# Kernel tuning notes

Measured on AMD Instinct MI355X. Metric: run time of the kernel, lower is better.

The kernel has to match this reference:

```python
import jax, jax.numpy as jnp
import numpy as np
from jax import lax

NUM_HEADS = 8
EPS = 1e-12  # F.normalize default eps


def setup_inputs() -> dict:
    key = jax.random.key(0)
    k1, k2, k3, k4 = jax.random.split(key, 4)
    b, c, h, w, d = 2, 128, 48, 48, 48
    x = jax.random.normal(k1, (b, c, h, w, d), dtype=jnp.float32)
    qkv_w = jax.random.normal(k2, (3 * c, c), dtype=jnp.float32) * 0.05
    dw_w = jax.random.normal(k3, (3 * c, 1, 3, 3, 3), dtype=jnp.float32) * 0.05
    proj_w = jax.random.normal(k4, (c, c), dtype=jnp.float32) * 0.05
    temperature = jnp.ones((1, NUM_HEADS, 1, 1), dtype=jnp.float32)
    return {"x": x, "qkv_w": qkv_w, "dw_w": dw_w, "proj_w": proj_w,
            "temperature": temperature}


def _l2_normalize(t):
    # F.normalize(t, dim=-1): t / max(||t||_2, eps)
    n = jnp.sqrt(jnp.sum(t * t, axis=-1, keepdims=True))
    return t / jnp.maximum(n, EPS)


def reference(x, qkv_w, dw_w, proj_w, temperature):
    b, c, h, w, d = x.shape
    dh = c // NUM_HEADS
    N = h * w * d
    # 1x1x1 pointwise conv (c -> 3c), no bias: pure channel GEMM
    qkv = jnp.einsum('oc,bchwd->bohwd', qkv_w, x)
    # depthwise 3x3x3 conv, padding=1, groups=3c
    qkv = lax.conv_general_dilated(
        qkv, dw_w, window_strides=(1, 1, 1), padding=[(1, 1)] * 3,
        dimension_numbers=('NCDHW', 'OIDHW', 'NCDHW'),
        feature_group_count=3 * c)
    q, k, v = jnp.split(qkv, 3, axis=1)
    q = q.reshape(b, NUM_HEADS, dh, N)
    k = k.reshape(b, NUM_HEADS, dh, N)
    v = v.reshape(b, NUM_HEADS, dh, N)
    q = _l2_normalize(q)
    k = _l2_normalize(k)
    # transposed attention: [b,H,dh,dh] score matrix over channels
    attn = jnp.einsum('bhin,bhjn->bhij', q, k) * temperature
    attn = jax.nn.softmax(attn, axis=-1)
    out = jnp.einsum('bhij,bhjn->bhin', attn, v).reshape(b, c, h, w, d)
    # 1x1x1 projection (c -> c), no bias
    return jnp.einsum('oc,bchwd->bohwd', proj_w, out)
```

## Files before the change

### kernel.cpp

```cpp
#include <hip/hip_runtime.h>
#include <hip/hip_bf16.h>
#include <stdint.h>
#include <stddef.h>

#define NSP 110592
#define SD  48
#define SD2 2304
#define CIN 128
#define C3  384
#define NH  8
#define NB  2
#define NQ  84934656ull

typedef __hip_bfloat16 bf16;
typedef __bf16 bf16x8 __attribute__((ext_vector_type(8)));
typedef float  f32x4  __attribute__((ext_vector_type(4)));

#define WOFF_QKVW 0
#define WOFF_DWW  49152
#define WOFF_PROJ 59520
#define WOFF_TEMP 75904
#define WTOTAL    75912

__device__ __forceinline__ float ldb(const bf16* p){ return __bfloat162float(*p); }
__device__ __forceinline__ float b2f(uint16_t u){
    union { float f; uint32_t i; } x; x.i = (uint32_t)u << 16; return x.f;
}
__device__ __forceinline__ uint16_t f2b(float f){
    bf16 h = __float2bfloat16(f); return *(uint16_t*)&h;
}

__global__ void k_sniff(const uint16_t* __restrict__ x16, int* __restrict__ flag)
{
    int t = threadIdx.x; int cnt = 0;
    for (int i = 0; i < 16; ++i) {
        uint16_t b = x16[(size_t)(t * 16 + i) * 2];
        int e = (b >> 7) & 0xFF;
        if (e >= 100 && e <= 140) ++cnt;
    }
    for (int off = 32; off; off >>= 1) cnt += __shfl_down(cnt, off, 64);
    __shared__ int s[4];
    if ((t & 63) == 0) s[t >> 6] = cnt;
    __syncthreads();
    if (t == 0) *flag = (s[0] + s[1] + s[2] + s[3] < 2048) ? 1 : 0;
}

__global__ void k_cvtw(const void* __restrict__ qw, const void* __restrict__ dw,
                       const void* __restrict__ pw, const void* __restrict__ tw,
                       bf16* __restrict__ wbuf, const int* __restrict__ flagp)
{
    int f = *flagp;
    int idx = blockIdx.x * 256 + threadIdx.x;
    if (idx >= WTOTAL) return;
    const void* src; int off;
    if (idx < WOFF_DWW)      { src = qw; off = idx; }
    else if (idx < WOFF_PROJ){ src = dw; off = idx - WOFF_DWW; }
    else if (idx < WOFF_TEMP){ src = pw; off = idx - WOFF_PROJ; }
    else                     { src = tw; off = idx - WOFF_TEMP; }
    float v = f ? ((const float*)src)[off]
                : __bfloat162float(((const bf16*)src)[off]);
    wbuf[idx] = __float2bfloat16(v);
}

__global__ __launch_bounds__(256) void k_transpose(const void* __restrict__ xin,
                                                   bf16* __restrict__ xT,
                                                   const int* __restrict__ flagp)
{
    int f = *flagp;
    int b = blockIdx.y;
    size_t tid = (size_t)blockIdx.x * 256 + threadIdx.x;
    int c = (int)(tid & 127);
    size_t n8 = tid >> 7;
    size_t base = ((size_t)b * CIN + c) * NSP + n8 * 8;
    bf16 pv[8];
    if (f) {
        const float* src = (const float*)xin + base;
        float4 a = *(const float4*)src;
        float4 d = *(const float4*)(src + 4);
        pv[0] = __float2bfloat16(a.x); pv[1] = __float2bfloat16(a.y);
        pv[2] = __float2bfloat16(a.z); pv[3] = __float2bfloat16(a.w);
        pv[4] = __float2bfloat16(d.x); pv[5] = __float2bfloat16(d.y);
        pv[6] = __float2bfloat16(d.z); pv[7] = __float2bfloat16(d.w);
    } else {
        uint4 v = *(const uint4*)((const bf16*)xin + base);
        const bf16* q = (const bf16*)&v;
#pragma unroll
        for (int j = 0; j < 8; ++j) pv[j] = q[j];
    }
    bf16* dst = xT + ((size_t)b * NSP + n8 * 8) * CIN + c;
#pragma unroll
    for (int j = 0; j < 8; ++j) dst[(size_t)j * CIN] = pv[j];
}

__global__ __launch_bounds__(256) void k_gemm_bt(const bf16* __restrict__ A,
                                                 const bf16* __restrict__ BT,
                                                 void* __restrict__ Cout,
                                                 int Mtotal,
                                                 const int* __restrict__ flagp,
                                                 int mblocks)
{
    __shared__ __align__(16) bf16 lA[128 * CIN];
    __shared__ __align__(16) bf16 lB[128 * CIN];
    int b = blockIdx.z;
    int bx = blockIdx.x;
    int mb, nb;
    if (mblocks == 3) {
        int g = bx / 24, w = bx % 24;
        nb = g * 8 + (w & 7);
        mb = w >> 3;
    } else { mb = 0; nb = bx; }
    size_t nbase = (size_t)nb * 128;
    const bf16* gA = A + (size_t)mb * 128 * CIN;
    const bf16* gB = BT + ((size_t)b * NSP + nbase) * CIN;
    int t = threadIdx.x;
#pragma unroll
    for (int i = 0; i < 8; ++i) {
        int off = (i * 256 + t) * 8;
        *(uint4*)&lA[off] = *(const uint4*)&gA[off];
        *(uint4*)&lB[off] = *(const uint4*)&gB[off];
    }
    __syncthreads();

    int wave = t >> 6, lane = t & 63;
    int wm = (wave & 1) * 64, wn = (wave >> 1) * 64;
    int lr = lane & 15, lq = lane >> 4;
    f32x4 acc[4][4];
#pragma unroll
    for (int mi = 0; mi < 4; ++mi)
#pragma unroll
        for (int ni = 0; ni < 4; ++ni) acc[mi][ni] = (f32x4){0.f, 0.f, 0.f, 0.f};

#pragma unroll
    for (int ks = 0; ks < 4; ++ks) {
        int kof = ks * 32 + lq * 8;
        bf16x8 af[4], bfv[4];
#pragma unroll
        for (int mi = 0; mi < 4; ++mi)
            af[mi] = *(const bf16x8*)&lA[(wm + mi * 16 + lr) * CIN + kof];
#pragma unroll
        for (int ni = 0; ni < 4; ++ni)
            bfv[ni] = *(const bf16x8*)&lB[(wn + ni * 16 + lr) * CIN + kof];
#pragma unroll
        for (int mi = 0; mi < 4; ++mi)
#pragma unroll
            for (int ni = 0; ni < 4; ++ni)
                acc[mi][ni] = __builtin_amdgcn_mfma_f32_16x16x32_bf16(
                    af[mi], bfv[ni], acc[mi][ni], 0, 0, 0);
    }

    int f32o = flagp ? *flagp : 0;
    size_t cb = ((size_t)b * Mtotal + (size_t)mb * 128) * NSP + nbase;
    if (f32o) {
        float* Cb = (float*)Cout + cb;
#pragma unroll
        for (int mi = 0; mi < 4; ++mi)
#pragma unroll
            for (int ni = 0; ni < 4; ++ni)
#pragma unroll
                for (int r = 0; r < 4; ++r)
                    Cb[(size_t)(wm + mi * 16 + lq * 4 + r) * NSP + wn + ni * 16 + lr]
                        = acc[mi][ni][r];
    } else {
        bf16* Cb = (bf16*)Cout + cb;
#pragma unroll
        for (int mi = 0; mi < 4; ++mi)
#pragma unroll
            for (int ni = 0; ni < 4; ++ni)
#pragma unroll
                for (int r = 0; r < 4; ++r)
                    Cb[(size_t)(wm + mi * 16 + lq * 4 + r) * NSP + wn + ni * 16 + lr]
                        = __float2bfloat16(acc[mi][ni][r]);
    }
}

#define PLN 3200
__global__ __launch_bounds__(256) void k_dwconv(const bf16* __restrict__ qkv1,
                                                const bf16* __restrict__ dw,
                                                bf16* __restrict__ qkv2,
                                                float* __restrict__ sums)
{
    __shared__ __align__(16) bf16 lds[8 * PLN];
    __shared__ float red[4];
    int bc = blockIdx.x;
    int slab = blockIdx.y;
    int z0 = slab * 6;
    int ch = bc % C3;
    int t = threadIdx.x;
    const bf16* src = qkv1 + (size_t)bc * NSP;
    bf16* dst = qkv2 + (size_t)bc * NSP;

    float wgt[27];
#pragma unroll
    for (int i = 0; i < 27; ++i) wgt[i] = ldb(&dw[ch * 27 + i]);

#pragma unroll
    for (int i = 0; i < 13; ++i) {
        int idx = i * 256 + t;
        if (idx < 3200) *(uint4*)&lds[idx * 8] = (uint4){0, 0, 0, 0};
    }
    __syncthreads();

#pragma unroll
    for (int i = 0; i < 9; ++i) {
        int vidx = i * 256 + t;
        int p = vidx / 288;
        int r = vidx - p * 288;
        int y = r / 6;
        int dg = r - y * 6;
        int zp = z0 - 1 + p;
        if ((unsigned)zp < SD) {
            uint4 v = *(const uint4*)&src[(size_t)zp * SD2 + y * SD + dg * 8];
            *(uint4*)&lds[(p * PLN + (y + 1) * 64 + 8 + dg * 8)] = v;
        }
    }
    __syncthreads();

    float ssq = 0.f;
#pragma unroll 1
    for (int r = 0; r < 3; ++r) {
        int s = r * 256 + t;
        if (s < 576) {
            int y = s / 12;
            int c4 = (s - y * 12) * 4;
            float acc[6][4];
#pragma unroll
            for (int oz = 0; oz < 6; ++oz)
#pragma unroll
                for (int d = 0; d < 4; ++d) acc[oz][d] = 0.f;

#pragma unroll
            for (int pl = 0; pl < 8; ++pl) {
                const uint16_t* P =
                    (const uint16_t*)lds + pl * PLN + y * 64 + 8 + c4;
                float v[3][6];
#pragma unroll
                for (int dy = 0; dy < 3; ++dy) {
                    const uint16_t* R = P + dy * 64;
                    uint2 m = *(const uint2*)R;
                    v[dy][0] = b2f(R[-1]);
                    v[dy][1] = b2f((uint16_t)m.x);
                    v[dy][2] = b2f((uint16_t)(m.x >> 16));
                    v[dy][3] = b2f((uint16_t)m.y);
                    v[dy][4] = b2f((uint16_t)(m.y >> 16));
                    v[dy][5] = b2f(R[4]);
                }
                float p0[4] = {0.f,0.f,0.f,0.f};
                float p1[4] = {0.f,0.f,0.f,0.f};
                float p2[4] = {0.f,0.f,0.f,0.f};
#pragma unroll
                for (int dy = 0; dy < 3; ++dy)
#pragma unroll
                    for (int dd = 0; dd < 3; ++dd) {
                        float w0 = wgt[dy * 3 + dd];
                        float w1 = wgt[9 + dy * 3 + dd];
                        float w2 = wgt[18 + dy * 3 + dd];
#pragma unroll
                        for (int d = 0; d < 4; ++d) {
                            float xv = v[dy][d + dd];
                            if (pl <= 5)            p0[d] += w0 * xv;
                            if (pl >= 1 && pl <= 6) p1[d] += w1 * xv;
                            if (pl >= 2)            p2[d] += w2 * xv;
                        }
                    }
#pragma unroll
                for (int d = 0; d < 4; ++d) {
                    if (pl <= 5)            acc[pl][d]     += p0[d];
                    if (pl >= 1 && pl <= 6) acc[pl - 1][d] += p1[d];
                    if (pl >= 2)            acc[pl - 2][d] += p2[d];
                }
            }
#pragma unroll
            for (int oz = 0; oz < 6; ++oz) {
                uint16_t u0 = f2b(acc[oz][0]), u1 = f2b(acc[oz][1]);
                uint16_t u2 = f2b(acc[oz][2]), u3 = f2b(acc[oz][3]);
                uint2 o;
                o.x = (uint32_t)u0 | ((uint32_t)u1 << 16);
                o.y = (uint32_t)u2 | ((uint32_t)u3 << 16);
                *(uint2*)&dst[(size_t)(z0 + oz) * SD2 + y * SD + c4] = o;
#pragma unroll
                for (int d = 0; d < 4; ++d) ssq += acc[oz][d] * acc[oz][d];
            }
        }
    }

    for (int off = 32; off; off >>= 1) ssq += __shfl_down(ssq, off, 64);
    if ((t & 63) == 0) red[t >> 6] = ssq;
    __syncthreads();
    if (t == 0) atomicAdd(&sums[bc], red[0] + red[1] + red[2] + red[3]);
}

__global__ __launch_bounds__(256) void k_scores(const bf16* __restrict__ qkv2,
                                                float* __restrict__ scores)
{
    int b = blockIdx.z, h = blockIdx.y;
    const bf16* qb = qkv2 + ((size_t)b * C3 + h * 16) * NSP;
    const bf16* kb = qkv2 + ((size_t)b * C3 + 128 + h * 16) * NSP;
    int t = threadIdx.x, w = t >> 6, lane = t & 63;
    int m = lane & 15, q4 = lane >> 4;
    size_t n0 = (size_t)blockIdx.x * 1024 + (size_t)w * 256 + (size_t)q4 * 8;
    const bf16* qp = qb + (size_t)m * NSP + n0;
    const bf16* kp = kb + (size_t)m * NSP + n0;
    f32x4 acc = (f32x4){0.f, 0.f, 0.f, 0.f};
#pragma unroll
    for (int it = 0; it < 8; ++it) {
        bf16x8 a  = *(const bf16x8*)(qp + it * 32);
        bf16x8 bb = *(const bf16x8*)(kp + it * 32);
        acc = __builtin_amdgcn_mfma_f32_16x16x32_bf16(a, bb, acc, 0, 0, 0);
    }
    float* srow = scores + (size_t)(b * NH + h) * 256;
#pragma unroll
    for (int r = 0; r < 4; ++r)
        atomicAdd(&srow[(q4 * 4 + r) * 16 + m], acc[r]);
}

__global__ void k_softmax(const float* __restrict__ scores,
                          const float* __restrict__ sums,
                          const bf16* __restrict__ temp,
                          float* __restrict__ attn)
{
    int t = threadIdx.x;
    int h = (t >> 4) & 7, b = t >> 7;
    float tau = __bfloat162float(temp[h]);
    float invq = 1.f / fmaxf(sqrtf(sums[b * C3 + (t & 127)]), 1e-12f);
    const float* srow = scores + (size_t)t * 16;
    float s[16]; float mx = -3.4e38f;
#pragma unroll
    for (int j = 0; j < 16; ++j) {
        float invk = 1.f / fmaxf(sqrtf(sums[b * C3 + 128 + h * 16 + j]), 1e-12f);
        s[j] = srow[j] * invq * invk * tau;
        mx = fmaxf(mx, s[j]);
    }
    float sum = 0.f;
#pragma unroll
    for (int j = 0; j < 16; ++j) { s[j] = expf(s[j] - mx); sum += s[j]; }
    float inv = 1.f / sum;
    float* arow = attn + (size_t)t * 16;
#pragma unroll
    for (int j = 0; j < 16; ++j) arow[j] = s[j] * inv;
}

__global__ __launch_bounds__(256) void k_av(const bf16* __restrict__ qkv2,
                                            const float* __restrict__ attn,
                                            bf16* __restrict__ outT)
{
    int b = blockIdx.z, h = blockIdx.y;
    const bf16* vb = qkv2 + ((size_t)b * C3 + 256 + h * 16) * NSP;
    __shared__ float at[256];
    int t = threadIdx.x;
    {
        int i = t >> 4, j = t & 15;
        at[j * 16 + i] = attn[(size_t)(b * NH + h) * 256 + t];
    }
    __syncthreads();
    size_t n0 = (size_t)blockIdx.x * 1024 + (size_t)t * 4;
    float acc[16][4];
#pragma unroll
    for (int i = 0; i < 16; ++i)
#pragma unroll
        for (int k = 0; k < 4; ++k) acc[i][k] = 0.f;
#pragma unroll
    for (int j = 0; j < 16; ++j) {
        uint2 raw = *(const uint2*)&vb[(size_t)j * NSP + n0];
        const bf16* rp = (const bf16*)&raw;
        float vf[4];
#pragma unroll
        for (int k = 0; k < 4; ++k) vf[k] = ldb(&rp[k]);
#pragma unroll
        for (int i = 0; i < 16; ++i) {
            float wv = at[j * 16 + i];
#pragma unroll
            for (int k = 0; k < 4; ++k) acc[i][k] += wv * vf[k];
        }
    }
    bf16* ob = outT + ((size_t)b * NSP + n0) * CIN + h * 16;
#pragma unroll
    for (int k = 0; k < 4; ++k) {
        bf16 tmp[16];
#pragma unroll
        for (int i = 0; i < 16; ++i) tmp[i] = __float2bfloat16(acc[i][k]);
        *(uint4*)&ob[(size_t)k * CIN]     = *(uint4*)&tmp[0];
        *(uint4*)&ob[(size_t)k * CIN + 8] = *(uint4*)&tmp[8];
    }
}

extern "C" void kernel_launch(void* const* d_in, const int* in_sizes, int n_in,
                              void* d_out, int out_size, void* d_ws, size_t ws_size,
                              hipStream_t stream)
{
    const void *px = nullptr, *pq = nullptr, *pd = nullptr, *pp = nullptr, *pt = nullptr;
    for (int i = 0; i < n_in; ++i) {
        switch (in_sizes[i]) {
            case 28311552: px = d_in[i]; break;
            case 49152:    pq = d_in[i]; break;
            case 10368:    pd = d_in[i]; break;
            case 16384:    pp = d_in[i]; break;
            case 8:        pt = d_in[i]; break;
        }
    }
    const size_t required = NQ * 4 + (1u << 20);
    if (!px || !pq || !pd || !pp || !pt || ws_size < required) {
        (void)hipMemsetAsync(d_out, 0, (size_t)out_size * 2, stream);
        return;
    }

    char* ws = (char*)d_ws;
    bf16* qkv1 = (bf16*)ws;
    bf16* qkv2 = (bf16*)(ws + NQ * 2);
    char* small = ws + NQ * 4;
    int*   flag   = (int*)small;
    float* sums   = (float*)(small + 256);
    float* scores = (float*)(small + 8192);
    float* attn   = (float*)(small + 24576);
    bf16*  wbuf   = (bf16*)(small + 40960);
    bf16* xT   = qkv2;
    bf16* outT = qkv1;

    (void)hipMemsetAsync(small, 0, 40960, stream);
    k_sniff<<<1, 256, 0, stream>>>((const uint16_t*)px, flag);
    k_cvtw<<<(WTOTAL + 255) / 256, 256, 0, stream>>>(pq, pd, pp, pt, wbuf, flag);
    k_transpose<<<dim3(6912, NB), 256, 0, stream>>>(px, xT, flag);
    k_gemm_bt<<<dim3(864 * 3, 1, NB), 256, 0, stream>>>(
        wbuf + WOFF_QKVW, xT, qkv1, C3, nullptr, 3);
    k_dwconv<<<dim3(NB * C3, 8), 256, 0, stream>>>(qkv1, wbuf + WOFF_DWW, qkv2, sums);
    k_scores<<<dim3(108, NH, NB), 256, 0, stream>>>(qkv2, scores);
    k_softmax<<<1, 256, 0, stream>>>(scores, sums, wbuf + WOFF_TEMP, attn);
    k_av<<<dim3(108, NH, NB), 256, 0, stream>>>(qkv2, attn, outT);
    k_gemm_bt<<<dim3(864, 1, NB), 256, 0, stream>>>(
        wbuf + WOFF_PROJ, outT, d_out, CIN, flag, 1);
}
```

Before: 552.0 us.

## Rework depthwise conv with packed FMA, swizzled LDS, smaller z-slabs

```diff
diff --git a/kernel.cpp b/kernel.cpp
--- a/kernel.cpp
+++ b/kernel.cpp
@@ -15,6 +15,7 @@
 typedef __hip_bfloat16 bf16;
 typedef __bf16 bf16x8 __attribute__((ext_vector_type(8)));
 typedef float  f32x4  __attribute__((ext_vector_type(4)));
+typedef float  f32x2  __attribute__((ext_vector_type(2)));
 
 #define WOFF_QKVW 0
 #define WOFF_DWW  49152
@@ -28,6 +29,12 @@
 }
 __device__ __forceinline__ uint16_t f2b(float f){
     bf16 h = __float2bfloat16(f); return *(uint16_t*)&h;
+}
+__device__ __forceinline__ float blo(uint32_t u){
+    union { float f; uint32_t i; } x; x.i = u << 16; return x.f;
+}
+__device__ __forceinline__ float bhi(uint32_t u){
+    union { float f; uint32_t i; } x; x.i = u & 0xffff0000u; return x.f;
 }
 
 __global__ void k_sniff(const uint16_t* __restrict__ x16, int* __restrict__ flag)
@@ -174,16 +181,17 @@
 }
 
 #define PLN 3200
-__global__ __launch_bounds__(256) void k_dwconv(const bf16* __restrict__ qkv1,
-                                                const bf16* __restrict__ dw,
-                                                bf16* __restrict__ qkv2,
-                                                float* __restrict__ sums)
-{
-    __shared__ __align__(16) bf16 lds[8 * PLN];
+#define PLB 6400
+__global__ __launch_bounds__(256, 4) void k_dwconv(const bf16* __restrict__ qkv1,
+                                                   const bf16* __restrict__ dw,
+                                                   bf16* __restrict__ qkv2,
+                                                   float* __restrict__ sums)
+{
+    __shared__ __align__(16) bf16 lds[6 * PLN];
     __shared__ float red[4];
     int bc = blockIdx.x;
     int slab = blockIdx.y;
-    int z0 = slab * 6;
+    int z0 = slab * 4;
     int ch = bc % C3;
     int t = threadIdx.x;
     const bf16* src = qkv1 + (size_t)bc * NSP;
@@ -194,95 +202,112 @@
     for (int i = 0; i < 27; ++i) wgt[i] = ldb(&dw[ch * 27 + i]);
 
 #pragma unroll
-    for (int i = 0; i < 13; ++i) {
+    for (int i = 0; i < 10; ++i) {
         int idx = i * 256 + t;
-        if (idx < 3200) *(uint4*)&lds[idx * 8] = (uint4){0, 0, 0, 0};
-    }
-    __syncthreads();
-
-#pragma unroll
-    for (int i = 0; i < 9; ++i) {
+        if (idx < 2400) *(uint4*)&lds[idx * 8] = (uint4){0, 0, 0, 0};
+    }
+    __syncthreads();
+
+#pragma unroll
+    for (int i = 0; i < 7; ++i) {
         int vidx = i * 256 + t;
-        int p = vidx / 288;
-        int r = vidx - p * 288;
-        int y = r / 6;
-        int dg = r - y * 6;
-        int zp = z0 - 1 + p;
-        if ((unsigned)zp < SD) {
-            uint4 v = *(const uint4*)&src[(size_t)zp * SD2 + y * SD + dg * 8];
-            *(uint4*)&lds[(p * PLN + (y + 1) * 64 + 8 + dg * 8)] = v;
+        if (vidx < 1728) {
+            int p = vidx / 288;
+            int rr = vidx - p * 288;
+            int yy = rr / 6;
+            int dg = rr - yy * 6;
+            int zp = z0 - 1 + p;
+            if ((unsigned)zp < SD) {
+                uint4 v = *(const uint4*)&src[(size_t)zp * SD2 + yy * SD + dg * 8];
+                int ab = p * PLB + (yy + 1) * 128 + 16 + dg * 16;
+                ab ^= ((yy + 1) & 7) << 4;
+                *(uint4*)((char*)lds + ab) = v;
+            }
         }
     }
     __syncthreads();
 
-    float ssq = 0.f;
+    f32x2 ss2 = (f32x2){0.f, 0.f};
 #pragma unroll 1
-    for (int r = 0; r < 3; ++r) {
+    for (int r = 0; r < 2; ++r) {
         int s = r * 256 + t;
-        if (s < 576) {
-            int y = s / 12;
-            int c4 = (s - y * 12) * 4;
-            float acc[6][4];
-#pragma unroll
-            for (int oz = 0; oz < 6; ++oz)
-#pragma unroll
-                for (int d = 0; d < 4; ++d) acc[oz][d] = 0.f;
-
-#pragma unroll
-            for (int pl = 0; pl < 8; ++pl) {
-                const uint16_t* P =
-                    (const uint16_t*)lds + pl * PLN + y * 64 + 8 + c4;
-                float v[3][6];
+        if (s < 288) {
+            int y = s / 6;
+            int c8 = (s - y * 6) * 8;
+            int offL[3], offM[3], offR[3];
+#pragma unroll
+            for (int dy = 0; dy < 3; ++dy) {
+                int row = y + dy;
+                int sw = (row & 7) << 4;
+                int rb = row * 128 + 2 * c8;
+                offL[dy] = (rb + 12) ^ sw;
+                offM[dy] = (rb + 16) ^ sw;
+                offR[dy] = (rb + 32) ^ sw;
+            }
+            f32x2 acc2[4][4];
+#pragma unroll
+            for (int oz = 0; oz < 4; ++oz)
+#pragma unroll
+                for (int m = 0; m < 4; ++m) acc2[oz][m] = (f32x2){0.f, 0.f};
+
+            const char* ldsb = (const char*)lds;
+#pragma unroll
+            for (int pl = 0; pl < 6; ++pl) {
+                const char* Pb = ldsb + pl * PLB;
 #pragma unroll
                 for (int dy = 0; dy < 3; ++dy) {
-                    const uint16_t* R = P + dy * 64;
-                    uint2 m = *(const uint2*)R;
-                    v[dy][0] = b2f(R[-1]);
-                    v[dy][1] = b2f((uint16_t)m.x);
-                    v[dy][2] = b2f((uint16_t)(m.x >> 16));
-                    v[dy][3] = b2f((uint16_t)m.y);
-                    v[dy][4] = b2f((uint16_t)(m.y >> 16));
-                    v[dy][5] = b2f(R[4]);
-                }
-                float p0[4] = {0.f,0.f,0.f,0.f};
-                float p1[4] = {0.f,0.f,0.f,0.f};
-                float p2[4] = {0.f,0.f,0.f,0.f};
-#pragma unroll
-                for (int dy = 0; dy < 3; ++dy)
-#pragma unroll
-                    for (int dd = 0; dd < 3; ++dd) {
-                        float w0 = wgt[dy * 3 + dd];
-                        float w1 = wgt[9 + dy * 3 + dd];
-                        float w2 = wgt[18 + dy * 3 + dd];
-#pragma unroll
-                        for (int d = 0; d < 4; ++d) {
-                            float xv = v[dy][d + dd];
-                            if (pl <= 5)            p0[d] += w0 * xv;
-                            if (pl >= 1 && pl <= 6) p1[d] += w1 * xv;
-                            if (pl >= 2)            p2[d] += w2 * xv;
-                        }
+                    uint32_t Lw = *(const uint32_t*)(Pb + offL[dy]);
+                    uint4    Mw = *(const uint4*)   (Pb + offM[dy]);
+                    uint32_t Rw = *(const uint32_t*)(Pb + offR[dy]);
+                    f32x2 vb0 = (f32x2){blo(Mw.x), bhi(Mw.x)};
+                    f32x2 vb1 = (f32x2){blo(Mw.y), bhi(Mw.y)};
+                    f32x2 vb2 = (f32x2){blo(Mw.z), bhi(Mw.z)};
+                    f32x2 vb3 = (f32x2){blo(Mw.w), bhi(Mw.w)};
+                    f32x2 va0 = (f32x2){bhi(Lw),   blo(Mw.x)};
+                    f32x2 va1 = (f32x2){bhi(Mw.x), blo(Mw.y)};
+                    f32x2 va2 = (f32x2){bhi(Mw.y), blo(Mw.z)};
+                    f32x2 va3 = (f32x2){bhi(Mw.z), blo(Mw.w)};
+                    f32x2 va4 = (f32x2){bhi(Mw.w), blo(Rw)};
+#pragma unroll
+                    for (int wp = 0; wp < 3; ++wp) {
+                        int oz = pl - wp;
+                        if (oz < 0 || oz > 3) continue;
+                        int wb = wp * 9 + dy * 3;
+                        float w0 = wgt[wb], w1 = wgt[wb + 1], w2 = wgt[wb + 2];
+                        f32x2 w0p = (f32x2){w0, w0};
+                        f32x2 w1p = (f32x2){w1, w1};
+                        f32x2 w2p = (f32x2){w2, w2};
+                        acc2[oz][0] = __builtin_elementwise_fma(va0, w0p, acc2[oz][0]);
+                        acc2[oz][1] = __builtin_elementwise_fma(va1, w0p, acc2[oz][1]);
+                        acc2[oz][2] = __builtin_elementwise_fma(va2, w0p, acc2[oz][2]);
+                        acc2[oz][3] = __builtin_elementwise_fma(va3, w0p, acc2[oz][3]);
+                        acc2[oz][0] = __builtin_elementwise_fma(vb0, w1p, acc2[oz][0]);
+                        acc2[oz][1] = __builtin_elementwise_fma(vb1, w1p, acc2[oz][1]);
+                        acc2[oz][2] = __builtin_elementwise_fma(vb2, w1p, acc2[oz][2]);
+                        acc2[oz][3] = __builtin_elementwise_fma(vb3, w1p, acc2[oz][3]);
+                        acc2[oz][0] = __builtin_elementwise_fma(va1, w2p, acc2[oz][0]);
+                        acc2[oz][1] = __builtin_elementwise_fma(va2, w2p, acc2[oz][1]);
+                        acc2[oz][2] = __builtin_elementwise_fma(va3, w2p, acc2[oz][2]);
+                        acc2[oz][3] = __builtin_elementwise_fma(va4, w2p, acc2[oz][3]);
                     }
-#pragma unroll
-                for (int d = 0; d < 4; ++d) {
-                    if (pl <= 5)            acc[pl][d]     += p0[d];
-                    if (pl >= 1 && pl <= 6) acc[pl - 1][d] += p1[d];
-                    if (pl >= 2)            acc[pl - 2][d] += p2[d];
                 }
             }
 #pragma unroll
-            for (int oz = 0; oz < 6; ++oz) {
-                uint16_t u0 = f2b(acc[oz][0]), u1 = f2b(acc[oz][1]);
-                uint16_t u2 = f2b(acc[oz][2]), u3 = f2b(acc[oz][3]);
-                uint2 o;
-                o.x = (uint32_t)u0 | ((uint32_t)u1 << 16);
-                o.y = (uint32_t)u2 | ((uint32_t)u3 << 16);
-                *(uint2*)&dst[(size_t)(z0 + oz) * SD2 + y * SD + c4] = o;
-#pragma unroll
-                for (int d = 0; d < 4; ++d) ssq += acc[oz][d] * acc[oz][d];
+            for (int oz = 0; oz < 4; ++oz) {
+                uint4 o;
+                o.x = (uint32_t)f2b(acc2[oz][0].x) | ((uint32_t)f2b(acc2[oz][0].y) << 16);
+                o.y = (uint32_t)f2b(acc2[oz][1].x) | ((uint32_t)f2b(acc2[oz][1].y) << 16);
+                o.z = (uint32_t)f2b(acc2[oz][2].x) | ((uint32_t)f2b(acc2[oz][2].y) << 16);
+                o.w = (uint32_t)f2b(acc2[oz][3].x) | ((uint32_t)f2b(acc2[oz][3].y) << 16);
+                *(uint4*)&dst[(size_t)(z0 + oz) * SD2 + y * SD + c8] = o;
+#pragma unroll
+                for (int m = 0; m < 4; ++m)
+                    ss2 = __builtin_elementwise_fma(acc2[oz][m], acc2[oz][m], ss2);
             }
         }
     }
 
+    float ssq = ss2.x + ss2.y;
     for (int off = 32; off; off >>= 1) ssq += __shfl_down(ssq, off, 64);
     if ((t & 63) == 0) red[t >> 6] = ssq;
     __syncthreads();
@@ -421,7 +446,7 @@
     k_transpose<<<dim3(6912, NB), 256, 0, stream>>>(px, xT, flag);
     k_gemm_bt<<<dim3(864 * 3, 1, NB), 256, 0, stream>>>(
         wbuf + WOFF_QKVW, xT, qkv1, C3, nullptr, 3);
-    k_dwconv<<<dim3(NB * C3, 8), 256, 0, stream>>>(qkv1, wbuf + WOFF_DWW, qkv2, sums);
+    k_dwconv<<<dim3(NB * C3, 12), 256, 0, stream>>>(qkv1, wbuf + WOFF_DWW, qkv2, sums);
     k_scores<<<dim3(108, NH, NB), 256, 0, stream>>>(qkv2, scores);
     k_softmax<<<1, 256, 0, stream>>>(scores, sums, wbuf + WOFF_TEMP, attn);
     k_av<<<dim3(108, NH, NB), 256, 0, stream>>>(qkv2, attn, outT);
```

After: 588.8 us. 6.7% more time.

## Use direct global-to-LDS loads with compact unpadded plane layout in dwconv

Applied to the files above, without the earlier changes.

```diff
diff --git a/kernel.cpp b/kernel.cpp
--- a/kernel.cpp
+++ b/kernel.cpp
@@ -28,6 +28,11 @@
 }
 __device__ __forceinline__ uint16_t f2b(float f){
     bf16 h = __float2bfloat16(f); return *(uint16_t*)&h;
+}
+__device__ __forceinline__ void gload_lds16(const void* g, void* l){
+    __builtin_amdgcn_global_load_lds(
+        (const __attribute__((address_space(1))) void*)g,
+        (__attribute__((address_space(3))) void*)l, 16, 0, 0);
 }
 
 __global__ void k_sniff(const uint16_t* __restrict__ x16, int* __restrict__ flag)
@@ -173,13 +178,13 @@
     }
 }
 
-#define PLN 3200
-__global__ __launch_bounds__(256) void k_dwconv(const bf16* __restrict__ qkv1,
-                                                const bf16* __restrict__ dw,
-                                                bf16* __restrict__ qkv2,
-                                                float* __restrict__ sums)
-{
-    __shared__ __align__(16) bf16 lds[8 * PLN];
+#define PLE 2400
+__global__ __launch_bounds__(256, 4) void k_dwconv(const bf16* __restrict__ qkv1,
+                                                   const bf16* __restrict__ dw,
+                                                   bf16* __restrict__ qkv2,
+                                                   float* __restrict__ sums)
+{
+    __shared__ __align__(16) bf16 lds[16 + 8 * PLE];
     __shared__ float red[4];
     int bc = blockIdx.x;
     int slab = blockIdx.y;
@@ -193,24 +198,38 @@
 #pragma unroll
     for (int i = 0; i < 27; ++i) wgt[i] = ldb(&dw[ch * 27 + i]);
 
-#pragma unroll
-    for (int i = 0; i < 13; ++i) {
-        int idx = i * 256 + t;
-        if (idx < 3200) *(uint4*)&lds[idx * 8] = (uint4){0, 0, 0, 0};
-    }
-    __syncthreads();
-
-#pragma unroll
-    for (int i = 0; i < 9; ++i) {
-        int vidx = i * 256 + t;
-        int p = vidx / 288;
-        int r = vidx - p * 288;
-        int y = r / 6;
-        int dg = r - y * 6;
-        int zp = z0 - 1 + p;
-        if ((unsigned)zp < SD) {
-            uint4 v = *(const uint4*)&src[(size_t)zp * SD2 + y * SD + dg * 8];
-            *(uint4*)&lds[(p * PLN + (y + 1) * 64 + 8 + dg * 8)] = v;
+    if (t < 98) {
+        int e;
+        if (t == 0)       e = 0;
+        else if (t == 97) e = 8 + 8 * PLE;
+        else {
+            int j = t - 1;
+            int p = j / 12, r12 = j - p * 12;
+            int rr = r12 / 6, q = r12 - rr * 6;
+            e = 8 + p * PLE + rr * 2352 + q * 8;
+        }
+        *(uint4*)&lds[e] = (uint4){0, 0, 0, 0};
+    }
+    if (slab == 0 || slab == 7) {
+        int p = (slab == 0) ? 0 : 7;
+        bf16* pb = lds + 8 + p * PLE;
+        for (int k = t; k < 300; k += 256)
+            *(uint4*)&pb[k * 8] = (uint4){0, 0, 0, 0};
+    }
+
+    {
+        int w = t >> 6, lane = t & 63;
+#pragma unroll
+        for (int i = 0; i < 10; ++i) {
+            int g = w + i * 4;
+            int p = g / 5, c = g - p * 5;
+            int zp = z0 - 1 + p;
+            if ((unsigned)zp < SD) {
+                const bf16* ga = src + (size_t)zp * SD2 + c * 512 + lane * 8;
+                bf16* la = lds + 8 + p * PLE + 48 + c * 512 + lane * 8;
+                if (c < 4)              gload_lds16(ga, la);
+                else if (lane < 32)     gload_lds16(ga, la);
+            }
         }
     }
     __syncthreads();
@@ -231,18 +250,18 @@
 #pragma unroll
             for (int pl = 0; pl < 8; ++pl) {
                 const uint16_t* P =
-                    (const uint16_t*)lds + pl * PLN + y * 64 + 8 + c4;
+                    (const uint16_t*)lds + 8 + pl * PLE + y * 48 + c4;
                 float v[3][6];
 #pragma unroll
                 for (int dy = 0; dy < 3; ++dy) {
-                    const uint16_t* R = P + dy * 64;
+                    const uint16_t* R = P + dy * 48;
                     uint2 m = *(const uint2*)R;
-                    v[dy][0] = b2f(R[-1]);
+                    v[dy][0] = (c4 == 0)  ? 0.f : b2f(R[-1]);
                     v[dy][1] = b2f((uint16_t)m.x);
                     v[dy][2] = b2f((uint16_t)(m.x >> 16));
                     v[dy][3] = b2f((uint16_t)m.y);
                     v[dy][4] = b2f((uint16_t)(m.y >> 16));
-                    v[dy][5] = b2f(R[4]);
+                    v[dy][5] = (c4 == 44) ? 0.f : b2f(R[4]);
                 }
                 float p0[4] = {0.f,0.f,0.f,0.f};
                 float p1[4] = {0.f,0.f,0.f,0.f};
```

Measured after the change: 1.403 ms. 154% more time.

## Fuse input transpose and bf16 conversion into QKV GEMM tile loading

Applied to the files above, without the earlier changes.

```diff
diff --git a/kernel.cpp b/kernel.cpp
--- a/kernel.cpp
+++ b/kernel.cpp
@@ -62,34 +62,110 @@
     wbuf[idx] = __float2bfloat16(v);
 }
 
-__global__ __launch_bounds__(256) void k_transpose(const void* __restrict__ xin,
-                                                   bf16* __restrict__ xT,
-                                                   const int* __restrict__ flagp)
-{
+__global__ __launch_bounds__(256) void k_gemm_qkv(const bf16* __restrict__ A,
+                                                  const void* __restrict__ X,
+                                                  bf16* __restrict__ Cout,
+                                                  const int* __restrict__ flagp)
+{
+    __shared__ __align__(16) bf16 lA[128 * CIN];
+    __shared__ __align__(16) bf16 lB[128 * CIN];
     int f = *flagp;
-    int b = blockIdx.y;
-    size_t tid = (size_t)blockIdx.x * 256 + threadIdx.x;
-    int c = (int)(tid & 127);
-    size_t n8 = tid >> 7;
-    size_t base = ((size_t)b * CIN + c) * NSP + n8 * 8;
-    bf16 pv[8];
+    int b = blockIdx.z;
+    int bx = blockIdx.x;
+    int g = bx / 24, w = bx % 24;
+    int nb = g * 8 + (w & 7);
+    int mb = w >> 3;
+    size_t nbase = (size_t)nb * 128;
+    const bf16* gA = A + (size_t)mb * 128 * CIN;
+    int t = threadIdx.x;
+
+#pragma unroll
+    for (int i = 0; i < 8; ++i) {
+        int idx = i * 256 + t;
+        int r = idx >> 4, cc = idx & 15;
+        *(uint4*)&lA[r * CIN + cc * 8] = *(const uint4*)&gA[r * CIN + cc * 8];
+    }
+
+    int cq = t >> 5;
+    int nq = t & 31;
     if (f) {
-        const float* src = (const float*)xin + base;
-        float4 a = *(const float4*)src;
-        float4 d = *(const float4*)(src + 4);
-        pv[0] = __float2bfloat16(a.x); pv[1] = __float2bfloat16(a.y);
-        pv[2] = __float2bfloat16(a.z); pv[3] = __float2bfloat16(a.w);
-        pv[4] = __float2bfloat16(d.x); pv[5] = __float2bfloat16(d.y);
-        pv[6] = __float2bfloat16(d.z); pv[7] = __float2bfloat16(d.w);
+        const float* xb = (const float*)X + (size_t)b * CIN * NSP + nbase;
+#pragma unroll
+        for (int p = 0; p < 4; ++p) {
+            int c0 = p * 32 + cq * 4;
+            float4 rv[4];
+#pragma unroll
+            for (int r = 0; r < 4; ++r)
+                rv[r] = *(const float4*)&xb[(size_t)(c0 + r) * NSP + nq * 4];
+#pragma unroll
+            for (int e = 0; e < 4; ++e) {
+                ushort4 o;
+                o.x = f2b(((const float*)&rv[0])[e]);
+                o.y = f2b(((const float*)&rv[1])[e]);
+                o.z = f2b(((const float*)&rv[2])[e]);
+                o.w = f2b(((const float*)&rv[3])[e]);
+                *(ushort4*)&lB[(nq * 4 + e) * CIN + c0] = o;
+            }
+        }
     } else {
-        uint4 v = *(const uint4*)((const bf16*)xin + base);
-        const bf16* q = (const bf16*)&v;
-#pragma unroll
-        for (int j = 0; j < 8; ++j) pv[j] = q[j];
-    }
-    bf16* dst = xT + ((size_t)b * NSP + n8 * 8) * CIN + c;
-#pragma unroll
-    for (int j = 0; j < 8; ++j) dst[(size_t)j * CIN] = pv[j];
+        const bf16* xb = (const bf16*)X + (size_t)b * CIN * NSP + nbase;
+#pragma unroll
+        for (int p = 0; p < 4; ++p) {
+            int c0 = p * 32 + cq * 4;
+            uint2 rv[4];
+#pragma unroll
+            for (int r = 0; r < 4; ++r)
+                rv[r] = *(const uint2*)&xb[(size_t)(c0 + r) * NSP + nq * 4];
+#pragma unroll
+            for (int e = 0; e < 4; ++e) {
+                ushort4 o;
+                o.x = (uint16_t)(e < 2 ? (rv[0].x >> (e * 16)) : (rv[0].y >> ((e - 2) * 16)));
+                o.y = (uint16_t)(e < 2 ? (rv[1].x >> (e * 16)) : (rv[1].y >> ((e - 2) * 16)));
+                o.z = (uint16_t)(e < 2 ? (rv[2].x >> (e * 16)) : (rv[2].y >> ((e - 2) * 16)));
+                o.w = (uint16_t)(e < 2 ? (rv[3].x >> (e * 16)) : (rv[3].y >> ((e - 2) * 16)));
+                *(ushort4*)&lB[(nq * 4 + e) * CIN + c0] = o;
+            }
+        }
+    }
+    __syncthreads();
+
+    int wave = t >> 6, lane = t & 63;
+    int wm = (wave & 1) * 64, wn = (wave >> 1) * 64;
+    int lr = lane & 15, lq = lane >> 4;
+    f32x4 acc[4][4];
+#pragma unroll
+    for (int mi = 0; mi < 4; ++mi)
+#pragma unroll
+        for (int ni = 0; ni < 4; ++ni) acc[mi][ni] = (f32x4){0.f, 0.f, 0.f, 0.f};
+
+#pragma unroll
+    for (int ks = 0; ks < 4; ++ks) {
+        int kof = ks * 32 + lq * 8;
+        bf16x8 af[4], bfv[4];
+#pragma unroll
+        for (int mi = 0; mi < 4; ++mi)
+            af[mi] = *(const bf16x8*)&lA[(wm + mi * 16 + lr) * CIN + kof];
+#pragma unroll
+        for (int ni = 0; ni < 4; ++ni)
+            bfv[ni] = *(const bf16x8*)&lB[(wn + ni * 16 + lr) * CIN + kof];
+#pragma unroll
+        for (int mi = 0; mi < 4; ++mi)
+#pragma unroll
+            for (int ni = 0; ni < 4; ++ni)
+                acc[mi][ni] = __builtin_amdgcn_mfma_f32_16x16x32_bf16(
+                    af[mi], bfv[ni], acc[mi][ni], 0, 0, 0);
+    }
+
+    size_t cb = ((size_t)b * C3 + (size_t)mb * 128) * NSP + nbase;
+    bf16* Cb = Cout + cb;
+#pragma unroll
+    for (int mi = 0; mi < 4; ++mi)
+#pragma unroll
+        for (int ni = 0; ni < 4; ++ni)
+#pragma unroll
+            for (int r = 0; r < 4; ++r)
+                Cb[(size_t)(wm + mi * 16 + lq * 4 + r) * NSP + wn + ni * 16 + lr]
+                    = __float2bfloat16(acc[mi][ni][r]);
 }
 
 __global__ __launch_bounds__(256) void k_gemm_bt(const bf16* __restrict__ A,
@@ -412,15 +488,13 @@
     float* scores = (float*)(small + 8192);
     float* attn   = (float*)(small + 24576);
     bf16*  wbuf   = (bf16*)(small + 40960);
-    bf16* xT   = qkv2;
     bf16* outT = qkv1;
 
     (void)hipMemsetAsync(small, 0, 40960, stream);
     k_sniff<<<1, 256, 0, stream>>>((const uint16_t*)px, flag);
     k_cvtw<<<(WTOTAL + 255) / 256, 256, 0, stream>>>(pq, pd, pp, pt, wbuf, flag);
-    k_transpose<<<dim3(6912, NB), 256, 0, stream>>>(px, xT, flag);
-    k_gemm_bt<<<dim3(864 * 3, 1, NB), 256, 0, stream>>>(
-        wbuf + WOFF_QKVW, xT, qkv1, C3, nullptr, 3);
+    k_gemm_qkv<<<dim3(864 * 3, 1, NB), 256, 0, stream>>>(
+        wbuf + WOFF_QKVW, px, qkv1, flag);
     k_dwconv<<<dim3(NB * C3, 8), 256, 0, stream>>>(qkv1, wbuf + WOFF_DWW, qkv2, sums);
     k_scores<<<dim3(108, NH, NB), 256, 0, stream>>>(qkv2, scores);
     k_softmax<<<1, 256, 0, stream>>>(scores, sums, wbuf + WOFF_TEMP, attn);
```

Result: faster. 533.7 us (-3.3%).
